# Optimization experiments

Hardware: AMD Instinct MI355X
Metric: run time of the kernel (lower is better)

## Reference

```python
import jax, jax.numpy as jnp
import numpy as np

# dims: B jets, K routed slots per jet, S particles, D embed, E experts, H heads
B, K, S, D, E, H = 512, 2, 128, 128, 4, 8
F = 4 * D  # ffn_dim
MAXN = 1.0 - 1e-5  # Poincare ball (c=1) max norm for projx


def _n(x):
    return jnp.sqrt(jnp.clip(jnp.sum(x * x, axis=-1, keepdims=True), 1e-15))


def expmap0(u):
    n = _n(u)
    return jnp.tanh(n) * u / n


def logmap0(x):
    n = _n(x)
    return jnp.arctanh(jnp.minimum(n, MAXN)) * x / n


def projx(x):
    n = _n(x)
    return jnp.where(n > MAXN, x * (MAXN / n), x)


def mobius_add(x, y):
    xy = jnp.sum(x * y, axis=-1, keepdims=True)
    x2 = jnp.sum(x * x, axis=-1, keepdims=True)
    y2 = jnp.sum(y * y, axis=-1, keepdims=True)
    num = (1.0 + 2.0 * xy + y2) * x + (1.0 - x2) * y
    den = 1.0 + 2.0 * xy + x2 * y2
    return num / jnp.clip(den, 1e-15)


def layernorm(x, g, b):
    m = jnp.mean(x, axis=-1, keepdims=True)
    v = jnp.mean((x - m) ** 2, axis=-1, keepdims=True)
    return g * (x - m) / jnp.sqrt(v + 1e-5) + b


def man_linear(x, W, b):
    # Manifold_Linear: mobius matvec == expmap0(W @ logmap0(x)), then mobius bias, projx
    return projx(mobius_add(expmap0(logmap0(x) @ W.T), expmap0(b)))


def mob_relu(x):
    # Mob_Act(ReLU): expmap0(relu(logmap0(x)))
    return expmap0(jax.nn.relu(logmap0(x)))


def setup_inputs():
    key = jax.random.key(0)
    ks = jax.random.split(key, 16)
    features = expmap0(0.05 * jax.random.normal(ks[0], (B, K, S, D), jnp.float32))
    # K distinct expert ids per sample (original .nonzero().item() assumes uniqueness)
    expert_indices = jnp.argsort(jax.random.uniform(ks[1], (B, E)), axis=1)[:, :K].astype(jnp.int32)
    pm = jax.random.uniform(ks[2], (B, S)) < 0.2
    pm = pm.at[:, 0].set(False)  # keep at least one valid token per row
    w = lambda k, shp, sc: sc * jax.random.normal(k, shp, jnp.float32)
    s = 1.0 / np.sqrt(D)
    sf = 1.0 / np.sqrt(F)
    return dict(
        features=features, expert_indices=expert_indices, padding_mask=pm,
        ln1_g=jnp.ones((E, D)), ln1_b=jnp.zeros((E, D)),
        ln2_g=jnp.ones((E, D)), ln2_b=jnp.zeros((E, D)),
        wq=w(ks[3], (E, D, D), s), bq=w(ks[4], (E, D), 0.02),
        wk=w(ks[5], (E, D, D), s), bk=w(ks[6], (E, D), 0.02),
        wv=w(ks[7], (E, D, D), s), bv=w(ks[8], (E, D), 0.02),
        wo=w(ks[9], (E, D, D), s), bo=w(ks[10], (E, D), 0.02),
        fc1_w=w(ks[11], (E, F, D), s), fc1_b=w(ks[12], (E, F), 0.02),
        fc2_w=w(ks[13], (E, D, F), sf), fc2_b=w(ks[14], (E, D), 0.02),
    )


def _mha(x, Wq, bq, Wk, bk, Wv, bv, Wo, bo, pad_bias):
    b, s, d = x.shape
    hd = d // H
    q = logmap0(man_linear(x, Wq, bq)).reshape(b, s, H, hd)
    k = logmap0(man_linear(x, Wk, bk)).reshape(b, s, H, hd)
    v = logmap0(man_linear(x, Wv, bv)).reshape(b, s, H, hd)
    scores = jnp.einsum('bqhd,bkhd->bhqk', q, k) * (1.0 / np.sqrt(hd)) + pad_bias
    att = jax.nn.softmax(scores, axis=-1)
    ctx = jnp.einsum('bhqk,bkhd->bqhd', att, v).reshape(b, s, d)
    return man_linear(expmap0(ctx), Wo, bo)


def _expert(x, e, P, pad_bias):
    res = x
    h = expmap0(layernorm(logmap0(x), P['ln1_g'][e], P['ln1_b'][e]))
    h = projx(_mha(h, P['wq'][e], P['bq'][e], P['wk'][e], P['bk'][e],
                   P['wv'][e], P['bv'][e], P['wo'][e], P['bo'][e], pad_bias))
    x = projx(mobius_add(h, res))
    res = x
    h = projx(expmap0(layernorm(logmap0(x), P['ln2_g'][e], P['ln2_b'][e])))
    h = projx(mob_relu(man_linear(h, P['fc1_w'][e], P['fc1_b'][e])))
    h = mob_relu(man_linear(h, P['fc2_w'][e], P['fc2_b'][e]))
    return projx(mobius_add(h, res))


def reference(features, expert_indices, padding_mask,
              ln1_g, ln1_b, ln2_g, ln2_b,
              wq, bq, wk, bk, wv, bv, wo, bo,
              fc1_w, fc1_b, fc2_w, fc2_b):
    P = dict(ln1_g=ln1_g, ln1_b=ln1_b, ln2_g=ln2_g, ln2_b=ln2_b,
             wq=wq, bq=bq, wk=wk, bk=bk, wv=wv, bv=bv, wo=wo, bo=bo,
             fc1_w=fc1_w, fc1_b=fc1_b, fc2_w=fc2_w, fc2_b=fc2_b)
    pad_bias = jnp.where(padding_mask, -1e9, 0.0)[:, None, None, :]  # [B,1,1,S]
    outs = []
    for e in range(E):  # small fixed expert loop (distinct params)
        sel = expert_indices == e  # [B,K]
        present = jnp.any(sel, axis=1)  # [B]
        slot = jnp.argmax(sel, axis=1)  # [B]
        x = jnp.take_along_axis(features, slot[:, None, None, None], axis=1)[:, 0]  # [B,S,D]
        y = _expert(x, e, P, pad_bias)
        outs.append(jnp.where(present[:, None, None], y, 0.0))
    return jnp.stack(outs, axis=1)  # [B,E,S,D]; zero rows where expert not routed
```

## Files before the change

kernel.cpp:

```cpp
#include <hip/hip_runtime.h>
#include <stdint.h>

#define SS 128
#define DD 128
#define EE 4
#define HH 8
#define HDIM 16
#define FF 512
#define BB 512
#define KK 2
#define NTASK (BB*KK)
#define MAXNF 0.99999f
#define NW3 786432

typedef unsigned short u16;
typedef unsigned int u32;

typedef __attribute__((ext_vector_type(8))) short s8v;
typedef __attribute__((ext_vector_type(4))) float f4v;

#define MFMA32(a,b,c) __builtin_amdgcn_mfma_f32_16x16x32_bf16(a,b,c,0,0,0)

__device__ __forceinline__ float bf2f(u16 h){ return __uint_as_float(((u32)h)<<16); }
__device__ __forceinline__ u16 f2bf(float f){
  u32 x = __float_as_uint(f);
  u32 r = x + 0x7FFFu + ((x>>16)&1u);
  return (u16)(r>>16);
}
__device__ __forceinline__ float bfl(u32 u){ return __uint_as_float(u<<16); }
__device__ __forceinline__ float bfh(u32 u){ return __uint_as_float(u & 0xFFFF0000u); }

__device__ __forceinline__ float wsum(float v){
  #pragma unroll
  for(int off=32; off>0; off>>=1) v += __shfl_xor(v, off, 64);
  return v;
}
__device__ __forceinline__ float wmax(float v){
  #pragma unroll
  for(int off=32; off>0; off>>=1) v = fmaxf(v, __shfl_xor(v, off, 64));
  return v;
}
__device__ __forceinline__ float artanhf_(float x){ return 0.5f*logf((1.f+x)/(1.f-x)); }

__device__ __forceinline__ u32 cvtpk(float a, float b){
  u32 r; asm("v_cvt_pk_bf16_f32 %0, %1, %2" : "=v"(r) : "v"(a), "v"(b)); return r;
}
__device__ __forceinline__ void split2(float a, float b, u32& H, u32& M, u32& L){
  H = cvtpk(a,b);
  float ra = a - bfl(H), rb = b - bfh(H);
  M = cvtpk(ra,rb);
  float sa = ra - bfl(M), sb = rb - bfh(M);
  L = cvtpk(sa,sb);
}
__device__ __forceinline__ void split8(const float* v, s8v& H, s8v& M, s8v& L){
  union { u32 w[4]; s8v s; } uh, um, ul;
  #pragma unroll
  for(int p=0;p<4;++p){
    u32 a,bq2,c; split2(v[2*p], v[2*p+1], a, bq2, c);
    uh.w[p]=a; um.w[p]=bq2; ul.w[p]=c;
  }
  H=uh.s; M=um.s; L=ul.s;
}
__device__ __forceinline__ s8v sel8(int c, s8v a, s8v b){ return c ? a : b; }

template<typename T> __device__ __forceinline__ float ldv(const T* p){
  if constexpr (sizeof(T)==2) return bf2f(*(const u16*)p);
  else return *(const float*)p;
}
template<typename T> __device__ __forceinline__ void stv(T* p, float v){
  if constexpr (sizeof(T)==2) *(u16*)p = f2bf(v);
  else *(float*)p = v;
}
template<typename T> __device__ __forceinline__ void loadrow(const T* p, float* w){
  if constexpr (sizeof(T)==2){
    const uint4* q=(const uint4*)p;
    #pragma unroll
    for(int r=0;r<16;++r){
      uint4 t=q[r];
      w[r*8+0]=bfl(t.x); w[r*8+1]=bfh(t.x);
      w[r*8+2]=bfl(t.y); w[r*8+3]=bfh(t.y);
      w[r*8+4]=bfl(t.z); w[r*8+5]=bfh(t.z);
      w[r*8+6]=bfl(t.w); w[r*8+7]=bfh(t.w);
    }
  } else {
    const float4* q=(const float4*)p;
    #pragma unroll
    for(int r=0;r<32;++r){ float4 t=q[r]; w[r*4]=t.x; w[r*4+1]=t.y; w[r*4+2]=t.z; w[r*4+3]=t.w; }
  }
}
__device__ __forceinline__ float dotrow(const float* __restrict__ w, const float* __restrict__ u){
  float a0=0.f,a1=0.f,a2=0.f,a3=0.f;
  #pragma unroll
  for(int i=0;i<128;i+=4){
    a0+=w[i]*u[i]; a1+=w[i+1]*u[i+1]; a2+=w[i+2]*u[i+2]; a3+=w[i+3]*u[i+3];
  }
  return (a0+a1)+(a2+a3);
}

template<int NPL> __device__ __forceinline__ float vnorm(const float* v){
  float s=0.f;
  #pragma unroll
  for(int i=0;i<NPL;++i) s += v[i]*v[i];
  s = wsum(s);
  return sqrtf(fmaxf(s, 1e-15f));
}
template<int NPL> __device__ __forceinline__ void f_logmap0(float* v){
  float n = vnorm<NPL>(v);
  float sc = artanhf_(fminf(n, MAXNF))/n;
  #pragma unroll
  for(int i=0;i<NPL;++i) v[i]*=sc;
}
template<int NPL> __device__ __forceinline__ void f_expmap0(float* v){
  float n = vnorm<NPL>(v);
  float sc = tanhf(n)/n;
  #pragma unroll
  for(int i=0;i<NPL;++i) v[i]*=sc;
}
template<int NPL> __device__ __forceinline__ void f_projx(float* v){
  float n = vnorm<NPL>(v);
  if(n > MAXNF){
    float sc = MAXNF/n;
    #pragma unroll
    for(int i=0;i<NPL;++i) v[i]*=sc;
  }
}
template<int NPL> __device__ __forceinline__ void f_mobius_add(float* x, const float* y){
  float xy=0.f, x2=0.f, y2=0.f;
  #pragma unroll
  for(int i=0;i<NPL;++i){ xy+=x[i]*y[i]; x2+=x[i]*x[i]; y2+=y[i]*y[i]; }
  xy=wsum(xy); x2=wsum(x2); y2=wsum(y2);
  float cx = 1.f + 2.f*xy + y2;
  float cy = 1.f - x2;
  float den = fmaxf(1.f + 2.f*xy + x2*y2, 1e-15f);
  float inv = 1.f/den;
  #pragma unroll
  for(int i=0;i<NPL;++i) x[i] = (cx*x[i] + cy*y[i])*inv;
}
template<int NPL> __device__ __forceinline__ void f_layernorm(float* v, const float* g, const float* b){
  const float invD = 1.f/(float)(NPL*64);
  float m=0.f;
  #pragma unroll
  for(int i=0;i<NPL;++i) m += v[i];
  m = wsum(m)*invD;
  float s2=0.f;
  #pragma unroll
  for(int i=0;i<NPL;++i){ v[i]-=m; s2 += v[i]*v[i]; }
  s2 = wsum(s2)*invD;
  float inv = 1.f/sqrtf(s2+1e-5f);
  #pragma unroll
  for(int i=0;i<NPL;++i) v[i] = g[i]*(v[i]*inv) + b[i];
}

__device__ __forceinline__ u32 xf32(int row, int colf){
  return (u32)row*512u + (((u32)colf*4u) ^ (((u32)row&7u)<<4));
}
__device__ __forceinline__ u32 xbh(int row, int colb){
  return (u32)row*256u + (((u32)colb*2u) ^ (((u32)row&7u)<<4));
}
__device__ __forceinline__ u32 xhid(int row, int colb){
  return (u32)row*1024u + (((u32)colb*2u) ^ (((u32)row&7u)<<4));
}
__device__ __forceinline__ u32 xfr_(int row, int colf){
  return (u32)row*2048u + (((u32)colf*4u) ^ (((u32)row&7u)<<4));
}

__global__ void prep_kernel(const u16* __restrict__ feat16,
                            const unsigned char* __restrict__ mask,
                            float* __restrict__ mbias, int* __restrict__ flag){
  __shared__ int s_stats, s_max, s_nan;
  if(threadIdx.x==0){ s_stats=0; s_max=0; s_nan=0; }
  __syncthreads();
  int c=0;
  for(int i=threadIdx.x; i<131072; i+=blockDim.x){
    u16 v = feat16[i];
    if(((v>>7)&0xFFu)==0xFFu) c++;
  }
  if(c) atomicAdd(&s_nan, c);
  int lstats=0, lmax=0;
  for(int i=threadIdx.x; i<BB*SS; i+=blockDim.x){
    int v = mask[i];
    if(v){
      lmax = v>lmax ? v : lmax;
      if((i&3)==1) lstats|=1;
      if((i&3)!=0) lstats|=2;
    }
  }
  if(lstats) atomicOr(&s_stats, lstats);
  atomicMax(&s_max, lmax);
  __syncthreads();
  if(threadIdx.x==0) *flag = (s_nan>0) ? 1 : 0;
  int mode;
  if(s_max<=1) mode = (s_stats&2) ? 0 : 1;
  else         mode = (s_stats&1) ? 2 : 3;
  for(int i=threadIdx.x; i<BB*SS; i+=blockDim.x){
    bool m2;
    if(mode==0)      m2 = mask[i]!=0;
    else if(mode==1) m2 = ((const int*)mask)[i]!=0;
    else if(mode==2) m2 = ((const u16*)mask)[i]!=0;
    else             m2 = ((((const u32*)mask)[i])<<1)!=0;
    mbias[i] = m2 ? -1e9f : 0.f;
  }
}

template<typename T>
__global__ void zero_nr(const int* __restrict__ flag, const int* __restrict__ eidx, T* __restrict__ out){
  const int want = (sizeof(T)==4) ? 1 : 0;
  if(*flag != want) return;
  for(int slab=blockIdx.x; slab<BB*EE; slab+=gridDim.x){
    int b = slab>>2, e = slab&3;
    if(eidx[b*KK]==e || eidx[b*KK+1]==e) continue;
    T* p = out + (size_t)slab*(SS*DD);
    for(int i=threadIdx.x; i<SS*DD; i+=blockDim.x){
      if constexpr (sizeof(T)==2) p[i] = (T)0; else p[i] = 0.f;
    }
  }
}

__global__ void wsplit_kernel(const int* __restrict__ flag,
                              const float* __restrict__ wq, const float* __restrict__ wk,
                              const float* __restrict__ wv, const float* __restrict__ wo,
                              const float* __restrict__ f1w, const float* __restrict__ f2w,
                              u16* __restrict__ wsp){
  if(*flag != 1) return;
  int i = blockIdx.x*256 + threadIdx.x;
  if(i >= NW3) return;
  float x;
  if(i < 65536)       x = wq[i];
  else if(i < 131072) x = wk[i-65536];
  else if(i < 196608) x = wv[i-131072];
  else if(i < 262144) x = wo[i-196608];
  else if(i < 524288) x = f1w[i-262144];
  else                x = f2w[i-524288];
  u32 H,M,L; split2(x,x,H,M,L);
  wsp[i]         = (u16)H;
  wsp[NW3 + i]   = (u16)M;
  wsp[2*NW3 + i] = (u16)L;
}

__global__ __launch_bounds__(512)
void moe_f32(const int* __restrict__ flag,
             const float* __restrict__ feat, const int* __restrict__ eidx,
             const float* __restrict__ mbias,
             const float* __restrict__ ln1g, const float* __restrict__ ln1b,
             const float* __restrict__ ln2g, const float* __restrict__ ln2b,
             const float* __restrict__ bq, const float* __restrict__ bk_,
             const float* __restrict__ bv, const float* __restrict__ bo,
             const float* __restrict__ f1b, const float* __restrict__ f2b,
             const u16* __restrict__ wsp,
             float* __restrict__ out, float* __restrict__ wsl, int ntask)
{
  if(*flag != 1) return;

  __shared__ __align__(16) char LB[163840];
  char* Uh = LB;
  char* Um = LB + 32768;
  char* R2 = LB + 65536;
  char* SX = LB + 131072;
  char* HB = LB + 98304;
  char* C2 = LB + 147456;

  const int tid = threadIdx.x;
  const int lane = tid & 63;
  const int w    = tid >> 6;
  const int ll   = lane & 15;
  const int hl   = lane >> 4;

  u16* myl = (u16*)wsl + (size_t)blockIdx.x * 16384;

  for(int task = blockIdx.x; task < ntask; task += gridDim.x){
    __syncthreads();
    const int b = task >> 1, slot = task & 1;
    const int e  = eidx[b*KK + slot];
    const int eo = eidx[b*KK + (slot^1)];
    int used = (1<<e)|(1<<eo), sp = 0, cnt = 0;
    #pragma unroll
    for(int t2=0;t2<4;++t2){ if(!((used>>t2)&1)){ if(cnt==slot) sp=t2; cnt++; } }
    const float* X = feat + (size_t)task * (SS*DD);
    float* own   = out + ((size_t)(b*EE+e )) * (SS*DD);
    float* spare = out + ((size_t)(b*EE+sp)) * (SS*DD);

    float g1[2],b1[2],g2[2],b2[2],ebq[2],ebk[2],ebv[2],ebo[2],ebf2[2],ebf1[8];
    {
      float2 t0;
      t0 = *(const float2*)(ln1g + e*DD + 2*lane); g1[0]=t0.x; g1[1]=t0.y;
      t0 = *(const float2*)(ln1b + e*DD + 2*lane); b1[0]=t0.x; b1[1]=t0.y;
      t0 = *(const float2*)(ln2g + e*DD + 2*lane); g2[0]=t0.x; g2[1]=t0.y;
      t0 = *(const float2*)(ln2b + e*DD + 2*lane); b2[0]=t0.x; b2[1]=t0.y;
      t0 = *(const float2*)(bq  + e*DD + 2*lane); ebq[0]=t0.x; ebq[1]=t0.y; f_expmap0<2>(ebq);
      t0 = *(const float2*)(bk_ + e*DD + 2*lane); ebk[0]=t0.x; ebk[1]=t0.y; f_expmap0<2>(ebk);
      t0 = *(const float2*)(bv  + e*DD + 2*lane); ebv[0]=t0.x; ebv[1]=t0.y; f_expmap0<2>(ebv);
      t0 = *(const float2*)(bo  + e*DD + 2*lane); ebo[0]=t0.x; ebo[1]=t0.y; f_expmap0<2>(ebo);
      t0 = *(const float2*)(f2b + e*DD + 2*lane); ebf2[0]=t0.x; ebf2[1]=t0.y; f_expmap0<2>(ebf2);
      #pragma unroll
      for(int j=0;j<4;++j){
        t0 = *(const float2*)(f1b + e*FF + 2*lane + 128*j); ebf1[2*j]=t0.x; ebf1[2*j+1]=t0.y;
      }
      f_expmap0<8>(ebf1);
    }
    float mb_reg[8];
    #pragma unroll
    for(int nt=0;nt<8;++nt) mb_reg[nt] = mbias[b*SS + nt*16 + ll];

    for(int r=0;r<16;++r){
      int t = w*16 + r;
      float2 xv = *(const float2*)(X + t*DD + 2*lane);
      float v[2] = {xv.x, xv.y};
      f_logmap0<2>(v);
      f_layernorm<2>(v, g1, b1);
      f_expmap0<2>(v);
      f_logmap0<2>(v);
      u32 H,M,L; split2(v[0],v[1],H,M,L);
      *(u32*)(Uh + xbh(t, 2*lane)) = H;
      *(u32*)(Um + xbh(t, 2*lane)) = M;
      ((u32*)myl)[t*64 + lane] = L;
    }
    __syncthreads();

    #pragma unroll
    for(int m=0;m<3;++m){
      const u32 tb = (m==0 ? 0u : (m==1 ? 65536u : 131072u)) + (u32)e*16384u;
      s8v Bh[8], Blm[8];
      {
        int nrow = w*16 + ll;
        #pragma unroll
        for(int c=0;c<8;++c){
          u32 koff = c*16 + (hl&1)*8;
          Bh[c]  = *(const s8v*)(wsp + 0*NW3 + tb + nrow*128 + koff);
          Blm[c] = *(const s8v*)(wsp + (hl<2?2:1)*NW3 + tb + nrow*128 + koff);
        }
      }
      for(int ch=0; ch<4; ++ch){
        #pragma unroll
        for(int sub=0; sub<2; ++sub){
          int mt = 2*ch + sub;
          f4v acc = {0.f,0.f,0.f,0.f};
          #pragma unroll
          for(int c=0;c<8;++c){
            int arow = mt*16 + ll;
            u32 koff = c*16 + (hl&1)*8;
            s8v A1 = *(const s8v*)((hl<2?Uh:Um) + xbh(arow, koff));
            s8v lf = *(const s8v*)((const u16*)myl + arow*128 + koff);
            s8v hf = *(const s8v*)(Uh + xbh(arow, koff));
            s8v A2 = sel8(hl<2, lf, hf);
            s8v B3 = sel8(hl<2, Bh[c], Blm[c]);
            acc = MFMA32(A1, Bh[c], acc);
            acc = MFMA32(A1, Blm[c], acc);
            acc = MFMA32(A2, B3, acc);
          }
          #pragma unroll
          for(int i=0;i<4;++i)
            *(float*)(SX + xf32(sub*16 + hl*4 + i, w*16 + ll)) = acc[i];
        }
        __syncthreads();
        for(int rr=0; rr<4; ++rr){
          int lr = w*4 + rr; int t = ch*32 + lr;
          float2 pp = *(const float2*)(SX + xf32(lr, 2*lane));
          float v[2] = {pp.x, pp.y};
          f_expmap0<2>(v);
          float eb[2];
          if(m==0){ eb[0]=ebq[0]; eb[1]=ebq[1]; }
          else if(m==1){ eb[0]=ebk[0]; eb[1]=ebk[1]; }
          else { eb[0]=ebv[0]; eb[1]=ebv[1]; }
          f_mobius_add<2>(v, eb);
          f_projx<2>(v);
          f_logmap0<2>(v);
          if(m==0){
            float2 o2; o2.x=v[0]; o2.y=v[1];
            *(float2*)(spare + t*DD + 2*lane) = o2;
          } else if(m==1){
            *(float*)(R2 + xf32(t, 2*lane))   = v[0];
            *(float*)(R2 + xf32(t, 2*lane+1)) = v[1];
          } else {
            own[(2*lane)*DD + t]   = v[0];
            own[(2*lane+1)*DD + t] = v[1];
          }
        }
        __syncthreads();
      }
    }

    for(int h=0; h<HH; ++h){
      {
        int tok = tid & 127, dq = tid >> 7;
        float4 vv = *(const float4*)(R2 + xf32(tok, h*16 + dq*4));
        u32 H0,M0,L0,H1,M1,L1;
        split2(vv.x,vv.y,H0,M0,L0); split2(vv.z,vv.w,H1,M1,L1);
        u32 o = (u32)tok*48u + (u32)dq*8u;
        *(u32*)(SX + 0*6144 + o) = H0; *(u32*)(SX + 0*6144 + o + 4) = H1;
        *(u32*)(SX + 1*6144 + o) = M0; *(u32*)(SX + 1*6144 + o + 4) = M1;
        *(u32*)(SX + 2*6144 + o) = L0; *(u32*)(SX + 2*6144 + o + 4) = L1;
      }
      __syncthreads();
      float qa[8];
      {
        float4 q0 = *(const float4*)(spare + (w*16+ll)*DD + h*16 + (hl&1)*8);
        float4 q1 = *(const float4*)(spare + (w*16+ll)*DD + h*16 + (hl&1)*8 + 4);
        qa[0]=q0.x; qa[1]=q0.y; qa[2]=q0.z; qa[3]=q0.w;
        qa[4]=q1.x; qa[5]=q1.y; qa[6]=q1.z; qa[7]=q1.w;
      }
      s8v QH,QM,QL; split8(qa, QH,QM,QL);
      s8v qA1 = sel8(hl<2, QH, QM);
      s8v qA2 = sel8(hl<2, QL, QH);
      f4v sc[8];
      #pragma unroll
      for(int nt=0;nt<8;++nt){
        u32 o = (u32)(nt*16+ll)*48u + (u32)(hl&1)*16u;
        s8v B1 = *(const s8v*)(SX + 0*6144 + o);
        s8v B2 = *(const s8v*)(SX + (hl<2?2:1)*6144 + o);
        s8v B3 = sel8(hl<2, B1, B2);
        f4v z = {0.f,0.f,0.f,0.f};
        z = MFMA32(qA1, B1, z);
        z = MFMA32(qA1, B2, z);
        z = MFMA32(qA2, B3, z);
        sc[nt] = z;
      }
      __syncthreads();
      #pragma unroll
      for(int i=0;i<4;++i){
        float p8[8]; float mx = -3e38f;
        #pragma unroll
        for(int nt=0;nt<8;++nt){ p8[nt] = sc[nt][i]*0.25f + mb_reg[nt]; mx = fmaxf(mx, p8[nt]); }
        #pragma unroll
        for(int o=1;o<16;o<<=1) mx = fmaxf(mx, __shfl_xor(mx, o, 64));
        float dn = 0.f;
        #pragma unroll
        for(int nt=0;nt<8;++nt){ p8[nt] = expf(p8[nt]-mx); dn += p8[nt]; }
        #pragma unroll
        for(int o=1;o<16;o<<=1) dn += __shfl_xor(dn, o, 64);
        float inv = 1.f/dn;
        #pragma unroll
        for(int nt=0;nt<8;++nt)
          *(float*)(LB + xf32(w*16 + hl*4 + i, nt*16 + ll)) = p8[nt]*inv;
      }
      f4v ca = {0.f,0.f,0.f,0.f};
      #pragma unroll
      for(int c=0;c<8;++c){
        float pa[8];
        {
          float4 p0 = *(const float4*)(LB + xf32(w*16+ll, c*16 + (hl&1)*8));
          float4 p1 = *(const float4*)(LB + xf32(w*16+ll, c*16 + (hl&1)*8 + 4));
          pa[0]=p0.x; pa[1]=p0.y; pa[2]=p0.z; pa[3]=p0.w;
          pa[4]=p1.x; pa[5]=p1.y; pa[6]=p1.z; pa[7]=p1.w;
        }
        s8v PH,PM,PL; split8(pa, PH,PM,PL);
        s8v pA1 = sel8(hl<2, PH, PM);
        s8v pA2 = sel8(hl<2, PL, PH);
        float va[8];
        {
          const float* vp = own + (h*16+ll)*DD + c*16 + (hl&1)*8;
          float4 v0 = *(const float4*)(vp);
          float4 v1 = *(const float4*)(vp + 4);
          va[0]=v0.x; va[1]=v0.y; va[2]=v0.z; va[3]=v0.w;
          va[4]=v1.x; va[5]=v1.y; va[6]=v1.z; va[7]=v1.w;
        }
        s8v VH,VM,VL; split8(va, VH,VM,VL);
        s8v vB2 = sel8(hl<2, VL, VM);
        s8v vB3 = sel8(hl<2, VH, VM);
        ca = MFMA32(pA1, VH, ca);
        ca = MFMA32(pA1, vB2, ca);
        ca = MFMA32(pA2, vB3, ca);
      }
      #pragma unroll
      for(int i=0;i<4;++i)
        *(float*)(R2 + xf32(w*16 + hl*4 + i, h*16 + ll)) = ca[i];
    }
    __syncthreads();

    for(int r=0;r<16;++r){
      int t = w*16 + r;
      float v[2];
      v[0] = *(const float*)(R2 + xf32(t, 2*lane));
      v[1] = *(const float*)(R2 + xf32(t, 2*lane+1));
      f_expmap0<2>(v);
      f_logmap0<2>(v);
      u32 H,M,L; split2(v[0],v[1],H,M,L);
      *(u32*)(Uh + xbh(t, 2*lane)) = H;
      *(u32*)(Um + xbh(t, 2*lane)) = M;
      ((u32*)myl)[t*64 + lane] = L;
    }
    __syncthreads();

    {
      const u32 tb = 196608u + (u32)e*16384u;
      s8v Bh[8], Blm[8];
      {
        int nrow = w*16 + ll;
        #pragma unroll
        for(int c=0;c<8;++c){
          u32 koff = c*16 + (hl&1)*8;
          Bh[c]  = *(const s8v*)(wsp + 0*NW3 + tb + nrow*128 + koff);
          Blm[c] = *(const s8v*)(wsp + (hl<2?2:1)*NW3 + tb + nrow*128 + koff);
        }
      }
      for(int ch=0; ch<4; ++ch){
        #pragma unroll
        for(int sub=0; sub<2; ++sub){
          int mt = 2*ch + sub;
          f4v acc = {0.f,0.f,0.f,0.f};
          #pragma unroll
          for(int c=0;c<8;++c){
            int arow = mt*16 + ll;
            u32 koff = c*16 + (hl&1)*8;
            s8v A1 = *(const s8v*)((hl<2?Uh:Um) + xbh(arow, koff));
            s8v lf = *(const s8v*)((const u16*)myl + arow*128 + koff);
            s8v hf = *(const s8v*)(Uh + xbh(arow, koff));
            s8v A2 = sel8(hl<2, lf, hf);
            s8v B3 = sel8(hl<2, Bh[c], Blm[c]);
            acc = MFMA32(A1, Bh[c], acc);
            acc = MFMA32(A1, Blm[c], acc);
            acc = MFMA32(A2, B3, acc);
          }
          #pragma unroll
          for(int i=0;i<4;++i)
            *(float*)(SX + xf32(sub*16 + hl*4 + i, w*16 + ll)) = acc[i];
        }
        __syncthreads();
        for(int rr=0; rr<4; ++rr){
          int lr = w*4 + rr; int t = ch*32 + lr;
          float2 pp = *(const float2*)(SX + xf32(lr, 2*lane));
          float v[2] = {pp.x, pp.y};
          f_expmap0<2>(v);
          f_mobius_add<2>(v, ebo);
          f_projx<2>(v);
          f_projx<2>(v);
          float2 rr2 = *(const float2*)(X + t*DD + 2*lane);
          float res[2] = {rr2.x, rr2.y};
          f_mobius_add<2>(v, res);
          f_projx<2>(v);
          float2 xo; xo.x=v[0]; xo.y=v[1];
          *(float2*)(own + t*DD + 2*lane) = xo;
          f_logmap0<2>(v);
          f_layernorm<2>(v, g2, b2);
          f_expmap0<2>(v);
          f_projx<2>(v);
          f_logmap0<2>(v);
          u32 H,M,L; split2(v[0],v[1],H,M,L);
          *(u32*)(Uh + xbh(t, 2*lane)) = H;
          *(u32*)(Um + xbh(t, 2*lane)) = M;
          ((u32*)myl)[t*64 + lane] = L;
        }
        __syncthreads();
      }
    }

    for(int tc=0; tc<8; ++tc){
      {
        f4v fa[4];
        #pragma unroll
        for(int n4=0;n4<4;++n4){ fa[n4][0]=0.f; fa[n4][1]=0.f; fa[n4][2]=0.f; fa[n4][3]=0.f; }
        #pragma unroll
        for(int c=0;c<8;++c){
          int arow = tc*16 + ll;
          u32 koff = c*16 + (hl&1)*8;
          s8v A1 = *(const s8v*)((hl<2?Uh:Um) + xbh(arow, koff));
          s8v lf = *(const s8v*)((const u16*)myl + arow*128 + koff);
          s8v hf = *(const s8v*)(Uh + xbh(arow, koff));
          s8v A2 = sel8(hl<2, lf, hf);
          #pragma unroll
          for(int n4=0;n4<4;++n4){
            u32 nrow = (u32)((w*4+n4)*16 + ll);
            s8v B1 = *(const s8v*)(wsp + 0*NW3 + 262144u + (u32)e*65536u + nrow*128 + koff);
            s8v B2 = *(const s8v*)(wsp + (hl<2?2:1)*NW3 + 262144u + (u32)e*65536u + nrow*128 + koff);
            s8v B3 = sel8(hl<2, B1, B2);
            fa[n4] = MFMA32(A1, B1, fa[n4]);
            fa[n4] = MFMA32(A1, B2, fa[n4]);
            fa[n4] = MFMA32(A2, B3, fa[n4]);
          }
        }
        #pragma unroll
        for(int n4=0;n4<4;++n4)
          #pragma unroll
          for(int i=0;i<4;++i)
            *(float*)(R2 + xfr_(hl*4+i, (w*4+n4)*16 + ll)) = fa[n4][i];
      }
      __syncthreads();
      for(int rr=0; rr<2; ++rr){
        int lr = w*2 + rr;
        float v[8];
        #pragma unroll
        for(int j=0;j<4;++j){
          float2 pp = *(const float2*)(R2 + xfr_(lr, 2*lane + 128*j));
          v[2*j]=pp.x; v[2*j+1]=pp.y;
        }
        f_expmap0<8>(v);
        f_mobius_add<8>(v, ebf1);
        f_projx<8>(v);
        f_logmap0<8>(v);
        #pragma unroll
        for(int i=0;i<8;++i) v[i] = fmaxf(v[i], 0.f);
        f_expmap0<8>(v);
        f_projx<8>(v);
        f_logmap0<8>(v);
        #pragma unroll
        for(int j=0;j<4;++j){
          u32 H,M,L; split2(v[2*j], v[2*j+1], H,M,L);
          *(u32*)(HB + 0*16384 + xhid(lr, 2*lane + 128*j)) = H;
          *(u32*)(HB + 1*16384 + xhid(lr, 2*lane + 128*j)) = M;
          *(u32*)(HB + 2*16384 + xhid(lr, 2*lane + 128*j)) = L;
        }
      }
      __syncthreads();
      {
        f4v ga = {0.f,0.f,0.f,0.f};
        #pragma unroll
        for(int c=0;c<32;++c){
          u32 koff = c*16 + (hl&1)*8;
          s8v A1 = *(const s8v*)(HB + (hl<2?0:1)*16384 + xhid(ll, koff));
          s8v lf = *(const s8v*)(HB + 2*16384 + xhid(ll, koff));
          s8v hf = *(const s8v*)(HB + 0*16384 + xhid(ll, koff));
          s8v A2 = sel8(hl<2, lf, hf);
          u32 nrow = (u32)(w*16 + ll);
          s8v B1 = *(const s8v*)(wsp + 0*NW3 + 524288u + (u32)e*65536u + nrow*512 + koff);
          s8v B2 = *(const s8v*)(wsp + (hl<2?2:1)*NW3 + 524288u + (u32)e*65536u + nrow*512 + koff);
          s8v B3 = sel8(hl<2, B1, B2);
          ga = MFMA32(A1, B1, ga);
          ga = MFMA32(A1, B2, ga);
          ga = MFMA32(A2, B3, ga);
        }
        #pragma unroll
        for(int i=0;i<4;++i)
          *(float*)(C2 + xf32(hl*4+i, w*16 + ll)) = ga[i];
      }
      __syncthreads();
      for(int rr=0; rr<2; ++rr){
        int lr = w*2 + rr; int gt = tc*16 + lr;
        float2 pp; pp.x = *(const float*)(C2 + xf32(lr, 2*lane));
        pp.y = *(const float*)(C2 + xf32(lr, 2*lane+1));
        float v[2] = {pp.x, pp.y};
        f_expmap0<2>(v);
        f_mobius_add<2>(v, ebf2);
        f_projx<2>(v);
        f_logmap0<2>(v);
        v[0]=fmaxf(v[0],0.f); v[1]=fmaxf(v[1],0.f);
        f_expmap0<2>(v);
        float2 xx = *(const float2*)(own + gt*DD + 2*lane);
        float x1v[2] = {xx.x, xx.y};
        f_mobius_add<2>(v, x1v);
        f_projx<2>(v);
        float2 o2; o2.x=v[0]; o2.y=v[1];
        *(float2*)(own + gt*DD + 2*lane) = o2;
      }
      __syncthreads();
    }

    {
      float4 z4 = {0.f,0.f,0.f,0.f};
      for(int i=tid; i<4096; i+=512) *(float4*)(spare + 4*i) = z4;
    }
  }
}

template<typename T>
__global__ __launch_bounds__(256)
void moe_kernel(const int* __restrict__ flag,
                const T* __restrict__ feat, const int* __restrict__ eidx,
                const float* __restrict__ mbias,
                const T* __restrict__ ln1g, const T* __restrict__ ln1b,
                const T* __restrict__ ln2g, const T* __restrict__ ln2b,
                const T* __restrict__ wq, const T* __restrict__ bq,
                const T* __restrict__ wk, const T* __restrict__ bk_,
                const T* __restrict__ wv, const T* __restrict__ bv,
                const T* __restrict__ wo, const T* __restrict__ bo,
                const T* __restrict__ f1w, const T* __restrict__ f1b,
                const T* __restrict__ f2w, const T* __restrict__ f2b,
                T* __restrict__ out, float* __restrict__ ws, int ntask)
{
  const int want = (sizeof(T)==4) ? 1 : 0;
  if(*flag != want) return;

  __shared__ float U[SS*DD];
  const int tid  = threadIdx.x;
  const int lane = tid & 63;
  const int wid  = tid >> 6;
  float* T0 = ws + (size_t)blockIdx.x * (4*SS*DD);
  float* T1 = T0 + SS*DD;
  float* T2 = T1 + SS*DD;
  float* T3 = T2 + SS*DD;

  for(int task = blockIdx.x; task < ntask; task += gridDim.x){
    __syncthreads();
    const int b = task >> 1;
    const int e = eidx[b*KK + (task & 1)];
    const T* X = feat + (size_t)task * (SS*DD);

    for(int r=0;r<32;++r){
      int t = wid*32 + r;
      float v[2];
      v[0]=ldv(&X[t*DD+lane]); v[1]=ldv(&X[t*DD+lane+64]);
      f_logmap0<2>(v);
      float g[2], bb[2];
      g[0]=ldv(&ln1g[e*DD+lane]);  g[1]=ldv(&ln1g[e*DD+lane+64]);
      bb[0]=ldv(&ln1b[e*DD+lane]); bb[1]=ldv(&ln1b[e*DD+lane+64]);
      f_layernorm<2>(v,g,bb);
      f_expmap0<2>(v);
      f_logmap0<2>(v);
      U[t*DD+lane]=v[0]; U[t*DD+lane+64]=v[1];
    }
    __syncthreads();

    {
      int j = tid & 127, tg = tid >> 7;
      for(int m=0;m<3;++m){
        const T* Wm = (m==0?wq : m==1?wk : wv) + (size_t)e*DD*DD + (size_t)j*DD;
        float* Ym = (m==0?T0 : m==1?T1 : T2);
        float w[128];
        loadrow(Wm, w);
        for(int tt=0;tt<64;++tt){
          int t = tg*64+tt;
          Ym[t*DD+j] = dotrow(w, &U[t*DD]);
        }
      }
    }
    __syncthreads();

    for(int m=0;m<3;++m){
      const T* bias = (m==0?bq : m==1?bk_ : bv) + e*DD;
      float* Y = (m==0?T0 : m==1?T1 : T2);
      for(int r=0;r<32;++r){
        int t = wid*32+r;
        float v[2]; v[0]=Y[t*DD+lane]; v[1]=Y[t*DD+lane+64];
        f_expmap0<2>(v);
        float ebv2[2]; ebv2[0]=ldv(&bias[lane]); ebv2[1]=ldv(&bias[lane+64]);
        f_expmap0<2>(ebv2);
        f_mobius_add<2>(v, ebv2);
        f_projx<2>(v);
        f_logmap0<2>(v);
        Y[t*DD+lane]=v[0]; Y[t*DD+lane+64]=v[1];
      }
    }
    __syncthreads();

    {
      const float* mb = mbias + b*SS;
      for(int h=0; h<HH; ++h){
        for(int r=0;r<32;++r){
          int t = wid*32+r;
          float q16[16];
          #pragma unroll
          for(int i=0;i<16;++i) q16[i] = T0[t*DD + h*HDIM + i];
          int k0 = lane, k1 = lane+64;
          float s0=0.f, s1=0.f;
          #pragma unroll
          for(int i=0;i<16;++i){
            s0 += q16[i]*T1[k0*DD + h*HDIM + i];
            s1 += q16[i]*T1[k1*DD + h*HDIM + i];
          }
          s0 = s0*0.25f + mb[k0];
          s1 = s1*0.25f + mb[k1];
          float mx = wmax(fmaxf(s0,s1));
          float p0 = expf(s0-mx), p1 = expf(s1-mx);
          float dn = wsum(p0+p1);
          p0 /= dn; p1 /= dn;
          float part[16];
          #pragma unroll
          for(int i=0;i<16;++i)
            part[i] = p0*T2[k0*DD+h*HDIM+i] + p1*T2[k1*DD+h*HDIM+i];
          #pragma unroll
          for(int off=1; off<64; off<<=1){
            #pragma unroll
            for(int i=0;i<16;++i) part[i] += __shfl_xor(part[i], off, 64);
          }
          if(lane==0){
            #pragma unroll
            for(int i=0;i<16;++i) T0[t*DD + h*HDIM + i] = part[i];
          }
        }
      }
    }
    __syncthreads();

    for(int r=0;r<32;++r){
      int t=wid*32+r;
      float v[2]; v[0]=T0[t*DD+lane]; v[1]=T0[t*DD+lane+64];
      f_expmap0<2>(v);
      f_logmap0<2>(v);
      U[t*DD+lane]=v[0]; U[t*DD+lane+64]=v[1];
    }
    __syncthreads();

    {
      int j=tid&127, tg=tid>>7;
      float w[128];
      loadrow(wo + (size_t)e*DD*DD + (size_t)j*DD, w);
      for(int tt=0;tt<64;++tt){
        int t=tg*64+tt;
        T1[t*DD+j] = dotrow(w, &U[t*DD]);
      }
    }
    __syncthreads();

    for(int r=0;r<32;++r){
      int t=wid*32+r;
      float v[2]; v[0]=T1[t*DD+lane]; v[1]=T1[t*DD+lane+64];
      f_expmap0<2>(v);
      float ebv2[2]; ebv2[0]=ldv(&bo[e*DD+lane]); ebv2[1]=ldv(&bo[e*DD+lane+64]);
      f_expmap0<2>(ebv2);
      f_mobius_add<2>(v, ebv2);
      f_projx<2>(v);
      f_projx<2>(v);
      float res[2]; res[0]=ldv(&X[t*DD+lane]); res[1]=ldv(&X[t*DD+lane+64]);
      f_mobius_add<2>(v, res);
      f_projx<2>(v);
      T3[t*DD+lane]=v[0]; T3[t*DD+lane+64]=v[1];
      f_logmap0<2>(v);
      float g2[2], b2[2];
      g2[0]=ldv(&ln2g[e*DD+lane]); g2[1]=ldv(&ln2g[e*DD+lane+64]);
      b2[0]=ldv(&ln2b[e*DD+lane]); b2[1]=ldv(&ln2b[e*DD+lane+64]);
      f_layernorm<2>(v,g2,b2);
      f_expmap0<2>(v);
      f_projx<2>(v);
      f_logmap0<2>(v);
      U[t*DD+lane]=v[0]; U[t*DD+lane+64]=v[1];
    }
    __syncthreads();

    float* HID = T0;
    for(int tc=0; tc<2; ++tc){
      for(int pass=0;pass<2;++pass){
        int f = pass*256 + tid;
        float w[128];
        loadrow(f1w + (size_t)e*FF*DD + (size_t)f*DD, w);
        for(int tt=0;tt<64;++tt){
          HID[tt*FF+f] = dotrow(w, &U[(tc*64+tt)*DD]);
        }
      }
      __syncthreads();
      for(int r=0;r<16;++r){
        int t = wid*16+r;
        float v[8];
        #pragma unroll
        for(int i=0;i<8;++i) v[i]=HID[t*FF+lane+64*i];
        f_expmap0<8>(v);
        float ebv8[8];
        #pragma unroll
        for(int i=0;i<8;++i) ebv8[i]=ldv(&f1b[e*FF+lane+64*i]);
        f_expmap0<8>(ebv8);
        f_mobius_add<8>(v, ebv8);
        f_projx<8>(v);
        f_logmap0<8>(v);
        #pragma unroll
        for(int i=0;i<8;++i) v[i]=fmaxf(v[i],0.f);
        f_expmap0<8>(v);
        f_projx<8>(v);
        f_logmap0<8>(v);
        #pragma unroll
        for(int i=0;i<8;++i) HID[t*FF+lane+64*i]=v[i];
      }
      __syncthreads();
      {
        int j=tid&127, tg=tid>>7;
        for(int fc=0;fc<4;++fc){
          float w[128];
          loadrow(f2w + (size_t)e*DD*FF + (size_t)j*FF + fc*128, w);
          for(int tt=0;tt<32;++tt){
            int t=tg*32+tt;
            float acc = dotrow(w, HID + t*FF + fc*128);
            if(fc==0) T2[t*DD+j]=acc; else T2[t*DD+j]+=acc;
          }
        }
      }
      __syncthreads();
      for(int r=0;r<16;++r){
        int t=wid*16+r; int gt = tc*64+t;
        float v[2]; v[0]=T2[t*DD+lane]; v[1]=T2[t*DD+lane+64];
        f_expmap0<2>(v);
        float ebv2[2]; ebv2[0]=ldv(&f2b[e*DD+lane]); ebv2[1]=ldv(&f2b[e*DD+lane+64]);
        f_expmap0<2>(ebv2);
        f_mobius_add<2>(v, ebv2);
        f_projx<2>(v);
        f_logmap0<2>(v);
        v[0]=fmaxf(v[0],0.f); v[1]=fmaxf(v[1],0.f);
        f_expmap0<2>(v);
        float x1v[2]; x1v[0]=T3[gt*DD+lane]; x1v[1]=T3[gt*DD+lane+64];
        f_mobius_add<2>(v, x1v);
        f_projx<2>(v);
        T* op = out + ((size_t)(b*EE+e)*SS + gt)*DD;
        stv(&op[lane],    v[0]);
        stv(&op[lane+64], v[1]);
      }
      __syncthreads();
    }
  }
}

extern "C" void kernel_launch(void* const* d_in, const int* in_sizes, int n_in,
                              void* d_out, int out_size, void* d_ws, size_t ws_size,
                              hipStream_t stream){
  const void* feat = d_in[0];
  const int* eidx = (const int*)d_in[1];
  const unsigned char* pmask = (const unsigned char*)d_in[2];
  float* ws = (float*)d_ws;

  int* flag = (int*)ws;
  float* mbias = ws + 16;
  float* tiles = ws + 16 + BB*SS;
  u16* wsp = (u16*)(ws + 16 + BB*SS);
  const size_t WSP_F32 = (size_t)(3*NW3)/2;
  float* wsl = ws + 16 + BB*SS + WSP_F32;

  long wsf = (long)(ws_size/sizeof(float));
  long avail_old = wsf - (16 + BB*SS);
  long remain = wsf - (long)(16 + BB*SS) - (long)WSP_F32;

  int G = (int)(avail_old / (long)(4*SS*DD));
  if(G > NTASK) G = NTASK;
  if(G < 1) G = 1;
  int G2 = (int)(remain / 8192);
  if(G2 > 256) G2 = 256;
  bool newpath = (G2 >= 1);

  prep_kernel<<<1,256,0,stream>>>((const u16*)feat, pmask, mbias, flag);
  zero_nr<u16>  <<<2048,256,0,stream>>>(flag, eidx, (u16*)d_out);
  zero_nr<float><<<2048,256,0,stream>>>(flag, eidx, (float*)d_out);

  if(newpath){
    wsplit_kernel<<<(NW3+255)/256,256,0,stream>>>(flag,
      (const float*)d_in[7], (const float*)d_in[9], (const float*)d_in[11], (const float*)d_in[13],
      (const float*)d_in[15], (const float*)d_in[17], wsp);
    moe_f32<<<G2,512,0,stream>>>(flag, (const float*)d_in[0], eidx, mbias,
      (const float*)d_in[3], (const float*)d_in[4], (const float*)d_in[5], (const float*)d_in[6],
      (const float*)d_in[8], (const float*)d_in[10], (const float*)d_in[12], (const float*)d_in[14],
      (const float*)d_in[16], (const float*)d_in[18],
      wsp, (float*)d_out, wsl, NTASK);
  }

  #define ARGS(T_) flag, (const T_*)d_in[0], eidx, mbias, \
    (const T_*)d_in[3], (const T_*)d_in[4], (const T_*)d_in[5], (const T_*)d_in[6], \
    (const T_*)d_in[7], (const T_*)d_in[8], (const T_*)d_in[9], (const T_*)d_in[10], \
    (const T_*)d_in[11], (const T_*)d_in[12], (const T_*)d_in[13], (const T_*)d_in[14], \
    (const T_*)d_in[15], (const T_*)d_in[16], (const T_*)d_in[17], (const T_*)d_in[18], \
    (T_*)d_out, tiles, NTASK
  moe_kernel<u16><<<G,256,0,stream>>>(ARGS(u16));
  if(!newpath){
    moe_kernel<float><<<G,256,0,stream>>>(ARGS(float));
  }
  #undef ARGS
}
```

Baseline: 4.289 ms.

## Sort tasks by expert and batch weight/operand loads ahead of MFMA loops

Adds a scheduling kernel that groups tasks by expert id, and assigns contiguous chunks of the sorted order to blocks by blockIdx modulo 8. The likely aim is to spread blocks on the same XCD over the same expert's weights so L2 reuse improves. It also hoists the low-part A loads, V loads and FC1/FC2 weight loads into register arrays before the MFMA chains, so more loads are in flight at once. The risks are higher register pressure and occupancy, and load imbalance when expert counts are uneven.

Result: slower. 4.633 ms (+8.0%).

```diff
diff --git a/kernel.cpp b/kernel.cpp
--- a/kernel.cpp
+++ b/kernel.cpp
@@ -237,6 +237,28 @@
   wsp[2*NW3 + i] = (u16)L;
 }
 
+__global__ void sched_kernel(const int* __restrict__ eidx, int* __restrict__ ord){
+  __shared__ int cnt[EE], base[EE], cur[EE];
+  int tid = threadIdx.x;
+  if(tid < EE) cnt[tid] = 0;
+  __syncthreads();
+  for(int t=tid; t<NTASK; t+=blockDim.x){
+    int b = t>>1; int e = eidx[b*KK + (t&1)];
+    atomicAdd(&cnt[e], 1);
+  }
+  __syncthreads();
+  if(tid==0){
+    int s=0;
+    for(int e2=0;e2<EE;++e2){ base[e2]=s; s+=cnt[e2]; cur[e2]=0; }
+  }
+  __syncthreads();
+  for(int t=tid; t<NTASK; t+=blockDim.x){
+    int b = t>>1; int e = eidx[b*KK + (t&1)];
+    int p = base[e] + atomicAdd(&cur[e], 1);
+    ord[p] = t;
+  }
+}
+
 __global__ __launch_bounds__(512)
 void moe_f32(const int* __restrict__ flag,
              const float* __restrict__ feat, const int* __restrict__ eidx,
@@ -246,7 +268,7 @@
              const float* __restrict__ bq, const float* __restrict__ bk_,
              const float* __restrict__ bv, const float* __restrict__ bo,
              const float* __restrict__ f1b, const float* __restrict__ f2b,
-             const u16* __restrict__ wsp,
+             const u16* __restrict__ wsp, const int* __restrict__ ord,
              float* __restrict__ out, float* __restrict__ wsl, int ntask)
 {
   if(*flag != 1) return;
@@ -267,8 +289,20 @@
 
   u16* myl = (u16*)wsl + (size_t)blockIdx.x * 16384;
 
-  for(int task = blockIdx.x; task < ntask; task += gridDim.x){
-    __syncthreads();
+  const int nb = gridDim.x;
+  int tstart, tend, tstep;
+  if(nb >= 8){
+    const int x = blockIdx.x & 7, j = blockIdx.x >> 3;
+    const int njx = (nb - x + 7) >> 3;
+    const int chunk = NTASK/8;
+    tstart = x*chunk + j; tend = (x+1)*chunk; tstep = njx;
+  } else {
+    tstart = blockIdx.x; tend = ntask; tstep = nb;
+  }
+
+  for(int ti = tstart; ti < tend; ti += tstep){
+    __syncthreads();
+    const int task = ord[ti];
     const int b = task >> 1, slot = task & 1;
     const int e  = eidx[b*KK + slot];
     const int eo = eidx[b*KK + (slot^1)];
@@ -292,8 +326,8 @@
       t0 = *(const float2*)(bo  + e*DD + 2*lane); ebo[0]=t0.x; ebo[1]=t0.y; f_expmap0<2>(ebo);
       t0 = *(const float2*)(f2b + e*DD + 2*lane); ebf2[0]=t0.x; ebf2[1]=t0.y; f_expmap0<2>(ebf2);
       #pragma unroll
-      for(int j=0;j<4;++j){
-        t0 = *(const float2*)(f1b + e*FF + 2*lane + 128*j); ebf1[2*j]=t0.x; ebf1[2*j+1]=t0.y;
+      for(int j2=0;j2<4;++j2){
+        t0 = *(const float2*)(f1b + e*FF + 2*lane + 128*j2); ebf1[2*j2]=t0.x; ebf1[2*j2+1]=t0.y;
       }
       f_expmap0<8>(ebf1);
     }
@@ -333,15 +367,18 @@
         #pragma unroll
         for(int sub=0; sub<2; ++sub){
           int mt = 2*ch + sub;
+          int arow = mt*16 + ll;
+          s8v lf8[8];
+          #pragma unroll
+          for(int c=0;c<8;++c)
+            lf8[c] = *(const s8v*)((const u16*)myl + arow*128 + c*16 + (hl&1)*8);
           f4v acc = {0.f,0.f,0.f,0.f};
           #pragma unroll
           for(int c=0;c<8;++c){
-            int arow = mt*16 + ll;
             u32 koff = c*16 + (hl&1)*8;
             s8v A1 = *(const s8v*)((hl<2?Uh:Um) + xbh(arow, koff));
-            s8v lf = *(const s8v*)((const u16*)myl + arow*128 + koff);
             s8v hf = *(const s8v*)(Uh + xbh(arow, koff));
-            s8v A2 = sel8(hl<2, lf, hf);
+            s8v A2 = sel8(hl<2, lf8[c], hf);
             s8v B3 = sel8(hl<2, Bh[c], Blm[c]);
             acc = MFMA32(A1, Bh[c], acc);
             acc = MFMA32(A1, Blm[c], acc);
@@ -434,31 +471,38 @@
       }
       f4v ca = {0.f,0.f,0.f,0.f};
       #pragma unroll
-      for(int c=0;c<8;++c){
-        float pa[8];
-        {
-          float4 p0 = *(const float4*)(LB + xf32(w*16+ll, c*16 + (hl&1)*8));
-          float4 p1 = *(const float4*)(LB + xf32(w*16+ll, c*16 + (hl&1)*8 + 4));
-          pa[0]=p0.x; pa[1]=p0.y; pa[2]=p0.z; pa[3]=p0.w;
-          pa[4]=p1.x; pa[5]=p1.y; pa[6]=p1.z; pa[7]=p1.w;
-        }
-        s8v PH,PM,PL; split8(pa, PH,PM,PL);
-        s8v pA1 = sel8(hl<2, PH, PM);
-        s8v pA2 = sel8(hl<2, PL, PH);
-        float va[8];
-        {
+      for(int grp=0; grp<2; ++grp){
+        float4 vv[8];
+        #pragma unroll
+        for(int cc=0; cc<4; ++cc){
+          int c = grp*4 + cc;
           const float* vp = own + (h*16+ll)*DD + c*16 + (hl&1)*8;
-          float4 v0 = *(const float4*)(vp);
-          float4 v1 = *(const float4*)(vp + 4);
-          va[0]=v0.x; va[1]=v0.y; va[2]=v0.z; va[3]=v0.w;
-          va[4]=v1.x; va[5]=v1.y; va[6]=v1.z; va[7]=v1.w;
-        }
-        s8v VH,VM,VL; split8(va, VH,VM,VL);
-        s8v vB2 = sel8(hl<2, VL, VM);
-        s8v vB3 = sel8(hl<2, VH, VM);
-        ca = MFMA32(pA1, VH, ca);
-        ca = MFMA32(pA1, vB2, ca);
-        ca = MFMA32(pA2, vB3, ca);
+          vv[2*cc]   = *(const float4*)(vp);
+          vv[2*cc+1] = *(const float4*)(vp + 4);
+        }
+        #pragma unroll
+        for(int cc=0; cc<4; ++cc){
+          int c = grp*4 + cc;
+          float pa[8];
+          {
+            float4 p0 = *(const float4*)(LB + xf32(w*16+ll, c*16 + (hl&1)*8));
+            float4 p1 = *(const float4*)(LB + xf32(w*16+ll, c*16 + (hl&1)*8 + 4));
+            pa[0]=p0.x; pa[1]=p0.y; pa[2]=p0.z; pa[3]=p0.w;
+            pa[4]=p1.x; pa[5]=p1.y; pa[6]=p1.z; pa[7]=p1.w;
+          }
+          s8v PH,PM,PL; split8(pa, PH,PM,PL);
+          s8v pA1 = sel8(hl<2, PH, PM);
+          s8v pA2 = sel8(hl<2, PL, PH);
+          float va[8];
+          va[0]=vv[2*cc].x; va[1]=vv[2*cc].y; va[2]=vv[2*cc].z; va[3]=vv[2*cc].w;
+          va[4]=vv[2*cc+1].x; va[5]=vv[2*cc+1].y; va[6]=vv[2*cc+1].z; va[7]=vv[2*cc+1].w;
+          s8v VH,VM,VL; split8(va, VH,VM,VL);
+          s8v vB2 = sel8(hl<2, VL, VM);
+          s8v vB3 = sel8(hl<2, VH, VM);
+          ca = MFMA32(pA1, VH, ca);
+          ca = MFMA32(pA1, vB2, ca);
+          ca = MFMA32(pA2, vB3, ca);
+        }
       }
       #pragma unroll
       for(int i=0;i<4;++i)
@@ -496,15 +540,18 @@
         #pragma unroll
         for(int sub=0; sub<2; ++sub){
           int mt = 2*ch + sub;
+          int arow = mt*16 + ll;
+          s8v lf8[8];
+          #pragma unroll
+          for(int c=0;c<8;++c)
+            lf8[c] = *(const s8v*)((const u16*)myl + arow*128 + c*16 + (hl&1)*8);
           f4v acc = {0.f,0.f,0.f,0.f};
           #pragma unroll
           for(int c=0;c<8;++c){
-            int arow = mt*16 + ll;
             u32 koff = c*16 + (hl&1)*8;
             s8v A1 = *(const s8v*)((hl<2?Uh:Um) + xbh(arow, koff));
-            s8v lf = *(const s8v*)((const u16*)myl + arow*128 + koff);
             s8v hf = *(const s8v*)(Uh + xbh(arow, koff));
-            s8v A2 = sel8(hl<2, lf, hf);
+            s8v A2 = sel8(hl<2, lf8[c], hf);
             s8v B3 = sel8(hl<2, Bh[c], Blm[c]);
             acc = MFMA32(A1, Bh[c], acc);
             acc = MFMA32(A1, Blm[c], acc);
@@ -545,27 +592,35 @@
 
     for(int tc=0; tc<8; ++tc){
       {
+        int arow = tc*16 + ll;
+        s8v lfT[8];
+        #pragma unroll
+        for(int c=0;c<8;++c)
+          lfT[c] = *(const s8v*)((const u16*)myl + arow*128 + c*16 + (hl&1)*8);
         f4v fa[4];
         #pragma unroll
-        for(int n4=0;n4<4;++n4){ fa[n4][0]=0.f; fa[n4][1]=0.f; fa[n4][2]=0.f; fa[n4][3]=0.f; }
-        #pragma unroll
-        for(int c=0;c<8;++c){
-          int arow = tc*16 + ll;
-          u32 koff = c*16 + (hl&1)*8;
-          s8v A1 = *(const s8v*)((hl<2?Uh:Um) + xbh(arow, koff));
-          s8v lf = *(const s8v*)((const u16*)myl + arow*128 + koff);
-          s8v hf = *(const s8v*)(Uh + xbh(arow, koff));
-          s8v A2 = sel8(hl<2, lf, hf);
-          #pragma unroll
-          for(int n4=0;n4<4;++n4){
-            u32 nrow = (u32)((w*4+n4)*16 + ll);
-            s8v B1 = *(const s8v*)(wsp + 0*NW3 + 262144u + (u32)e*65536u + nrow*128 + koff);
-            s8v B2 = *(const s8v*)(wsp + (hl<2?2:1)*NW3 + 262144u + (u32)e*65536u + nrow*128 + koff);
-            s8v B3 = sel8(hl<2, B1, B2);
-            fa[n4] = MFMA32(A1, B1, fa[n4]);
-            fa[n4] = MFMA32(A1, B2, fa[n4]);
-            fa[n4] = MFMA32(A2, B3, fa[n4]);
-          }
+        for(int n4=0;n4<4;++n4){
+          u32 nrow = (u32)((w*4+n4)*16 + ll);
+          s8v B1v[8], B2v[8];
+          #pragma unroll
+          for(int c=0;c<8;++c){
+            u32 koff = c*16 + (hl&1)*8;
+            B1v[c] = *(const s8v*)(wsp + 0*NW3 + 262144u + (u32)e*65536u + nrow*128 + koff);
+            B2v[c] = *(const s8v*)(wsp + (hl<2?2:1)*NW3 + 262144u + (u32)e*65536u + nrow*128 + koff);
+          }
+          f4v acc = {0.f,0.f,0.f,0.f};
+          #pragma unroll
+          for(int c=0;c<8;++c){
+            u32 koff = c*16 + (hl&1)*8;
+            s8v A1 = *(const s8v*)((hl<2?Uh:Um) + xbh(arow, koff));
+            s8v hf = *(const s8v*)(Uh + xbh(arow, koff));
+            s8v A2 = sel8(hl<2, lfT[c], hf);
+            s8v B3 = sel8(hl<2, B1v[c], B2v[c]);
+            acc = MFMA32(A1, B1v[c], acc);
+            acc = MFMA32(A1, B2v[c], acc);
+            acc = MFMA32(A2, B3, acc);
+          }
+          fa[n4] = acc;
         }
         #pragma unroll
         for(int n4=0;n4<4;++n4)
@@ -578,9 +633,9 @@
         int lr = w*2 + rr;
         float v[8];
         #pragma unroll
-        for(int j=0;j<4;++j){
-          float2 pp = *(const float2*)(R2 + xfr_(lr, 2*lane + 128*j));
-          v[2*j]=pp.x; v[2*j+1]=pp.y;
+        for(int j2=0;j2<4;++j2){
+          float2 pp = *(const float2*)(R2 + xfr_(lr, 2*lane + 128*j2));
+          v[2*j2]=pp.x; v[2*j2+1]=pp.y;
         }
         f_expmap0<8>(v);
         f_mobius_add<8>(v, ebf1);
@@ -592,30 +647,40 @@
         f_projx<8>(v);
         f_logmap0<8>(v);
         #pragma unroll
-        for(int j=0;j<4;++j){
-          u32 H,M,L; split2(v[2*j], v[2*j+1], H,M,L);
-          *(u32*)(HB + 0*16384 + xhid(lr, 2*lane + 128*j)) = H;
-          *(u32*)(HB + 1*16384 + xhid(lr, 2*lane + 128*j)) = M;
-          *(u32*)(HB + 2*16384 + xhid(lr, 2*lane + 128*j)) = L;
+        for(int j2=0;j2<4;++j2){
+          u32 H,M,L; split2(v[2*j2], v[2*j2+1], H,M,L);
+          *(u32*)(HB + 0*16384 + xhid(lr, 2*lane + 128*j2)) = H;
+          *(u32*)(HB + 1*16384 + xhid(lr, 2*lane + 128*j2)) = M;
+          *(u32*)(HB + 2*16384 + xhid(lr, 2*lane + 128*j2)) = L;
         }
       }
       __syncthreads();
       {
+        u32 nrow = (u32)(w*16 + ll);
         f4v ga = {0.f,0.f,0.f,0.f};
         #pragma unroll
-        for(int c=0;c<32;++c){
-          u32 koff = c*16 + (hl&1)*8;
-          s8v A1 = *(const s8v*)(HB + (hl<2?0:1)*16384 + xhid(ll, koff));
-          s8v lf = *(const s8v*)(HB + 2*16384 + xhid(ll, koff));
-          s8v hf = *(const s8v*)(HB + 0*16384 + xhid(ll, koff));
-          s8v A2 = sel8(hl<2, lf, hf);
-          u32 nrow = (u32)(w*16 + ll);
-          s8v B1 = *(const s8v*)(wsp + 0*NW3 + 524288u + (u32)e*65536u + nrow*512 + koff);
-          s8v B2 = *(const s8v*)(wsp + (hl<2?2:1)*NW3 + 524288u + (u32)e*65536u + nrow*512 + koff);
-          s8v B3 = sel8(hl<2, B1, B2);
-          ga = MFMA32(A1, B1, ga);
-          ga = MFMA32(A1, B2, ga);
-          ga = MFMA32(A2, B3, ga);
+        for(int grp=0; grp<4; ++grp){
+          s8v B1v[8], B2v[8];
+          #pragma unroll
+          for(int cc=0;cc<8;++cc){
+            int c = grp*8 + cc;
+            u32 koff = c*16 + (hl&1)*8;
+            B1v[cc] = *(const s8v*)(wsp + 0*NW3 + 524288u + (u32)e*65536u + nrow*512 + koff);
+            B2v[cc] = *(const s8v*)(wsp + (hl<2?2:1)*NW3 + 524288u + (u32)e*65536u + nrow*512 + koff);
+          }
+          #pragma unroll
+          for(int cc=0;cc<8;++cc){
+            int c = grp*8 + cc;
+            u32 koff = c*16 + (hl&1)*8;
+            s8v A1 = *(const s8v*)(HB + (hl<2?0:1)*16384 + xhid(ll, koff));
+            s8v lf = *(const s8v*)(HB + 2*16384 + xhid(ll, koff));
+            s8v hf = *(const s8v*)(HB + 0*16384 + xhid(ll, koff));
+            s8v A2 = sel8(hl<2, lf, hf);
+            s8v B3 = sel8(hl<2, B1v[cc], B2v[cc]);
+            ga = MFMA32(A1, B1v[cc], ga);
+            ga = MFMA32(A1, B2v[cc], ga);
+            ga = MFMA32(A2, B3, ga);
+          }
         }
         #pragma unroll
         for(int i=0;i<4;++i)
@@ -896,11 +961,12 @@
   float* tiles = ws + 16 + BB*SS;
   u16* wsp = (u16*)(ws + 16 + BB*SS);
   const size_t WSP_F32 = (size_t)(3*NW3)/2;
-  float* wsl = ws + 16 + BB*SS + WSP_F32;
+  int* ord = (int*)(ws + 16 + BB*SS + WSP_F32);
+  float* wsl = ws + 16 + BB*SS + WSP_F32 + 1024;
 
   long wsf = (long)(ws_size/sizeof(float));
   long avail_old = wsf - (16 + BB*SS);
-  long remain = wsf - (long)(16 + BB*SS) - (long)WSP_F32;
+  long remain = wsf - (long)(16 + BB*SS) - (long)WSP_F32 - 1024;
 
   int G = (int)(avail_old / (long)(4*SS*DD));
   if(G > NTASK) G = NTASK;
@@ -914,6 +980,7 @@
   zero_nr<float><<<2048,256,0,stream>>>(flag, eidx, (float*)d_out);
 
   if(newpath){
+    sched_kernel<<<1,256,0,stream>>>(eidx, ord);
     wsplit_kernel<<<(NW3+255)/256,256,0,stream>>>(flag,
       (const float*)d_in[7], (const float*)d_in[9], (const float*)d_in[11], (const float*)d_in[13],
       (const float*)d_in[15], (const float*)d_in[17], wsp);
@@ -921,7 +988,7 @@
       (const float*)d_in[3], (const float*)d_in[4], (const float*)d_in[5], (const float*)d_in[6],
       (const float*)d_in[8], (const float*)d_in[10], (const float*)d_in[12], (const float*)d_in[14],
       (const float*)d_in[16], (const float*)d_in[18],
-      wsp, (float*)d_out, wsl, NTASK);
+      wsp, ord, (float*)d_out, wsl, NTASK);
   }
 
   #define ARGS(T_) flag, (const T_*)d_in[0], eidx, mbias, \
```
